# Kernel tuning notes

Measured on AMD Instinct MI355X. Metric: run time of the kernel, lower is better.

The kernel has to match this reference:

```python
import jax, jax.numpy as jnp
import numpy as np

K = 16  # neighbors per point (init kwarg k)


def setup_inputs() -> dict:
    key = jax.random.key(0)
    k0, k1, k2 = jax.random.split(key, 3)
    B, N, C, L, O = 4, 8192, 32, 64, 128
    return {
        "x": jax.random.normal(k0, (B, N, C), dtype=jnp.float32),
        "W_lin": jax.random.normal(k1, (C, L), dtype=jnp.float32) * 0.1,
        "b_lin": jnp.zeros((L,), dtype=jnp.float32),
        "W_conv": jax.random.normal(k2, (L, O), dtype=jnp.float32) * 0.1,
        "b_conv": jnp.zeros((O,), dtype=jnp.float32),
    }


def reference(x, W_lin, b_lin, W_conv, b_conv):
    # --- knn(x, k): squared-euclidean pairwise distance + top-k nearest ---
    sq = jnp.sum(x * x, axis=-1)                                   # [B,N]
    # dist[b,i,j] = ||x_i - x_j||^2  (self included, dist 0)
    dist = sq[:, :, None] - 2.0 * jnp.einsum('bnc,bmc->bnm', x, x) + sq[:, None, :]
    _, idx = jax.lax.top_k(-dist, K)                               # [B,N,K] int32
    # --- index_points: gather neighbor features ---
    knn_x = jax.vmap(lambda xb, ib: xb[ib])(x, idx)                # [B,N,K,C]
    # --- max pool over neighbors ---
    pooled = jnp.max(knn_x, axis=2)                                # [B,N,C]
    # --- Dense(linear) -> Conv1D(out_channel, kernel_size=1) -> relu ---
    h = pooled @ W_lin + b_lin                                     # [B,N,64]
    h = h @ W_conv + b_conv                                        # [B,N,128]
    return jax.nn.relu(h)
```

## Files before the change

kernel.cpp:

```cpp
#include <hip/hip_runtime.h>

#define NPTS   8192
#define CCH    32
#define LDIM   64
#define ODIM   128
#define KNN    16
#define QPB    64
#define TILEC  128
#define NTIL   (NPTS / TILEC)
#define NBLK   ((4 * NPTS) / QPB)
#define SCAP   57
#define MARGIN 0.75f
#define T32STR 65

typedef _Float16 half8   __attribute__((ext_vector_type(8)));
typedef float    float4v __attribute__((ext_vector_type(4)));

#define LDS_BYTES 54016
#define OFF_SQ   8192
#define OFF_SL   34816
#define OFF_SC   49408
#define OFF_TQ   49664
#define OFF_KN   49920
#define OFF_HH   8704

__device__ __forceinline__ void gload_lds16(const void* g, void* l) {
    __builtin_amdgcn_global_load_lds(
        (const __attribute__((address_space(1))) unsigned int*)g,
        (__attribute__((address_space(3))) unsigned int*)l, 16, 0, 0);
}
__device__ __forceinline__ void gload_lds4(const void* g, void* l) {
    __builtin_amdgcn_global_load_lds(
        (const __attribute__((address_space(1))) unsigned int*)g,
        (__attribute__((address_space(3))) unsigned int*)l, 4, 0, 0);
}

__global__ __launch_bounds__(256)
void prep_kernel(const float* __restrict__ x, float* __restrict__ sqg,
                 _Float16* __restrict__ xh) {
    __shared__ float lx[128 * 33];
    const int r = blockIdx.x;
    const int t = threadIdx.x;
    const float* src = x + (size_t)r * 4096;

    #pragma unroll
    for (int i = 0; i < 4; ++i) {
        int f4 = t + i * 256;
        float4 v = ((const float4*)src)[f4];
        int f = f4 * 4, pt = f >> 5, ch = f & 31;
        float* d = lx + pt * 33 + ch;
        d[0] = v.x; d[1] = v.y; d[2] = v.z; d[3] = v.w;
    }
    __syncthreads();
    if (t < 128) {
        const float* row = lx + t * 33;
        float s = 0.f;
        #pragma unroll
        for (int k = 0; k < 8; ++k) {
            float a = row[4*k], b = row[4*k+1], c = row[4*k+2], d = row[4*k+3];
            s += a * a + b * b + c * c + d * d;
        }
        sqg[r * 128 + t] = s;
    }
    char* rec = (char*)xh + (size_t)r * 8192;
    #pragma unroll
    for (int i = 0; i < 2; ++i) {
        int s2 = t * 2 + i;
        int st = s2 >> 6, q = (s2 >> 4) & 3, col = s2 & 15;
        const float* row = lx + (st * 16 + col) * 33 + q * 8;
        half8 h;
        #pragma unroll
        for (int j = 0; j < 8; ++j) h[j] = (_Float16)row[j];
        *(half8*)(rec + s2 * 16) = h;
    }
}

__global__ __launch_bounds__(512, 4)
void graph_layer_kernel(const float* __restrict__ x,
                        const float* __restrict__ sqg,
                        const _Float16* __restrict__ xh,
                        const float* __restrict__ Wl,
                        const float* __restrict__ bl,
                        const float* __restrict__ Wc,
                        const float* __restrict__ bc,
                        float* __restrict__ out)
{
    __shared__ __align__(16) char smem[LDS_BYTES];
    int*   slist = (int*)(smem + OFF_SL);
    float* t32   = (float*)smem;
    int*   scnt  = (int*)(smem + OFF_SC);
    float* tq    = (float*)(smem + OFF_TQ);
    float* skeys = (float*)smem;
    int*   kn    = (int*)(smem + OFF_KN);
    float* pl    = (float*)smem;
    float* hh    = (float*)(smem + OFF_HH);

    const int tid  = threadIdx.x;
    const int lane = tid & 63;
    const int w    = tid >> 6;
    const int g    = w >> 2;
    const int lw   = w & 3;
    const int col  = lane & 15;
    const int quad = lane >> 4;
    const float INF = __builtin_inff();

    const int bid = blockIdx.x;
    const int xcd = bid & 7, ixc = bid >> 3;
    const int vb  = ((xcd >> 1) << 7) | ((xcd & 1) << 6) | ixc;

    const int qb0 = vb * QPB;
    const int b   = qb0 >> 13;
    const int qbl = qb0 & (NPTS - 1);
    const int S   = vb & 31;
    const float* xb  = x   + (size_t)(b << 13) * CCH;
    const float* sqb = sqg + (b << 13);
    const char*  xhb = (const char*)xh + (size_t)b * NTIL * 8192;

    half8 qh;
    {
        int p = qb0 + lw * 16 + col;
        qh = *(const half8*)((const char*)xh
              + (size_t)(p >> 7) * 8192 + ((p >> 4) & 7) * 1024
              + quad * 256 + (p & 15) * 16);
    }

    auto tileof = [&](int I) { return (((I + S) & 31) << 1) | g; };
    auto bufat  = [&](int I) { return smem + (((g << 1) | (I & 1)) * 8704); };

    auto stage = [&](int I) {
        char* sb = bufat(I);
        int tile = tileof(I);
        const char* src = xhb + (size_t)tile * 8192;
        int tg = tid & 255;
        gload_lds16(src + tg * 16,        sb + lw * 1024);
        gload_lds16(src + 4096 + tg * 16, sb + 4096 + lw * 1024);
        if (lw < 2)
            gload_lds4(sqb + tile * TILEC + lw * 64 + lane, sb + OFF_SQ + lw * 256);
    };

    float m1[4] = {INF, INF, INF, INF};
    float m2[4] = {INF, INF, INF, INF};

    stage(0);
    __syncthreads();
    #pragma unroll 1
    for (int I = 0; I < 32; ++I) {
        if (I + 1 < 32) stage(I + 1);
        const char*  cb = bufat(I);
        const float* sv = (const float*)(cb + OFF_SQ);
        #pragma unroll
        for (int st = 0; st < 8; ++st) {
            half8 bh = *(const half8*)(cb + st * 1024 + lane * 16);
            float sc = sv[st * 16 + col];
            float4v acc = __builtin_amdgcn_mfma_f32_16x16x32_f16(
                qh, bh, (float4v){0.f, 0.f, 0.f, 0.f}, 0, 0, 0);
            #pragma unroll
            for (int j = 0; j < 4; ++j) {
                float key = fmaf(-2.f, acc[j], sc);
                float o1  = m1[j];
                m1[j] = fminf(key, o1);
                m2[j] = __builtin_amdgcn_fmed3f(key, o1, m2[j]);
            }
        }
        __syncthreads();
    }

    #pragma unroll
    for (int j = 0; j < 4; ++j) {
        int qq = lw * 16 + quad * 4 + j;
        t32[qq * T32STR + g * 32 + col * 2 + 0] = m1[j];
        t32[qq * T32STR + g * 32 + col * 2 + 1] = m2[j];
    }
    __syncthreads();
    {
        int q  = tid & 63;
        int wt = tid >> 6;
        float v[8]; int r[8];
        #pragma unroll
        for (int u = 0; u < 8; ++u) { v[u] = t32[q * T32STR + wt * 8 + u]; r[u] = 0; }
        #pragma unroll 8
        for (int jj = 0; jj < 64; ++jj) {
            float vj = t32[q * T32STR + jj];
            #pragma unroll
            for (int u = 0; u < 8; ++u)
                r[u] += (int)(vj < v[u]) | ((int)(vj == v[u]) & (int)(jj < wt * 8 + u));
        }
        #pragma unroll
        for (int u = 0; u < 8; ++u)
            if (r[u] == KNN - 1) tq[q] = v[u];
        if (tid < QPB) scnt[tid] = 0;
    }
    __syncthreads();
    float T2[4];
    #pragma unroll
    for (int j = 0; j < 4; ++j) T2[j] = tq[lw * 16 + quad * 4 + j] + MARGIN;

    stage(0);
    __syncthreads();
    #pragma unroll 1
    for (int I = 0; I < 32; ++I) {
        if (I + 1 < 32) stage(I + 1);
        const char*  cb = bufat(I);
        const float* sv = (const float*)(cb + OFF_SQ);
        int tbase = tileof(I) * TILEC;
        #pragma unroll
        for (int st = 0; st < 8; ++st) {
            half8 bh = *(const half8*)(cb + st * 1024 + lane * 16);
            float sc = sv[st * 16 + col];
            float4v acc = __builtin_amdgcn_mfma_f32_16x16x32_f16(
                qh, bh, (float4v){0.f, 0.f, 0.f, 0.f}, 0, 0, 0);
            #pragma unroll
            for (int j = 0; j < 4; ++j) {
                float key = fmaf(-2.f, acc[j], sc);
                if (key < T2[j]) {
                    int qq = lw * 16 + quad * 4 + j;
                    int slot = atomicAdd(&scnt[qq], 1);
                    if (slot < SCAP)
                        slist[qq * SCAP + slot] = tbase + st * 16 + col;
                }
            }
        }
        __syncthreads();
    }

    {
        int qq = tid & 63, sb8 = tid >> 6;
        int n = scnt[qq]; if (n > SCAP) n = SCAP;
        const float4* xi4 = (const float4*)(xb + (size_t)(qbl + qq) * CCH);
        for (int s = sb8; s < n; s += 8) {
            int jdx = slist[qq * SCAP + s];
            const float4* xj = (const float4*)(xb + (size_t)jdx * CCH);
            float a0 = 0.f, a1 = 0.f, a2 = 0.f, a3 = 0.f;
            #pragma unroll 2
            for (int k = 0; k < 8; ++k) {
                float4 cv = xj[k], qv = xi4[k];
                a0 = fmaf(cv.x, qv.x, a0); a1 = fmaf(cv.y, qv.y, a1);
                a2 = fmaf(cv.z, qv.z, a2); a3 = fmaf(cv.w, qv.w, a3);
            }
            float dot = (a0 + a1) + (a2 + a3);
            skeys[qq * SCAP + s] = fmaf(-2.f, dot, sqb[jdx]);
        }
    }
    __syncthreads();
    {
        int q  = tid & 63;
        int wt = tid >> 6;
        int n = scnt[q]; if (n > SCAP) n = SCAP;
        for (int s = wt; s < n; s += 8) {
            float k = skeys[q * SCAP + s];
            int   i = slist[q * SCAP + s];
            int rank = 0;
            #pragma unroll 4
            for (int jj = 0; jj < n; ++jj) {
                float kj = skeys[q * SCAP + jj];
                int   ij = slist[q * SCAP + jj];
                rank += (int)(kj < k) | ((int)(kj == k) & (int)(ij < i));
            }
            if (rank < KNN) kn[q * KNN + rank] = i;
        }
    }
    __syncthreads();

    {
        int q = tid >> 3, part = tid & 7;
        float4 m0 = make_float4(-INF, -INF, -INF, -INF);
        #pragma unroll 4
        for (int k = 0; k < KNN; ++k) {
            int j = kn[q * KNN + k];
            float4 v = *(const float4*)(xb + (size_t)j * CCH + part * 4);
            m0.x = fmaxf(m0.x, v.x); m0.y = fmaxf(m0.y, v.y);
            m0.z = fmaxf(m0.z, v.z); m0.w = fmaxf(m0.w, v.w);
        }
        float* d = pl + q * 33 + part * 4;
        d[0] = m0.x; d[1] = m0.y; d[2] = m0.z; d[3] = m0.w;
    }
    __syncthreads();
    {
        int l = tid & 63, qg2 = tid >> 6;
        #pragma unroll 1
        for (int qq = qg2; qq < QPB; qq += 8) {
            float acc = bl[l];
            #pragma unroll 8
            for (int c = 0; c < CCH; ++c)
                acc = fmaf(pl[qq * 33 + c], Wl[c * LDIM + l], acc);
            hh[qq * 65 + l] = acc;
        }
    }
    __syncthreads();
    {
        int o = tid & 127, qh2 = tid >> 7;
        #pragma unroll 1
        for (int qq = qh2; qq < QPB; qq += 4) {
            float acc = bc[o];
            #pragma unroll 8
            for (int l = 0; l < LDIM; ++l)
                acc = fmaf(hh[qq * 65 + l], Wc[l * ODIM + o], acc);
            out[(size_t)(qb0 + qq) * ODIM + o] = fmaxf(acc, 0.f);
        }
    }
}

extern "C" void kernel_launch(void* const* d_in, const int* in_sizes, int n_in,
                              void* d_out, int out_size, void* d_ws, size_t ws_size,
                              hipStream_t stream) {
    const float* x  = (const float*)d_in[0];
    const float* Wl = (const float*)d_in[1];
    const float* bl = (const float*)d_in[2];
    const float* Wc = (const float*)d_in[3];
    const float* bc = (const float*)d_in[4];
    float* out = (float*)d_out;
    float*    sqf = (float*)d_ws;
    _Float16* xh  = (_Float16*)((char*)d_ws + 131072);
    (void)in_sizes; (void)n_in; (void)out_size; (void)ws_size;

    hipLaunchKernelGGL(prep_kernel, dim3(256), dim3(256), 0, stream, x, sqf, xh);
    hipLaunchKernelGGL(graph_layer_kernel, dim3(NBLK), dim3(512), 0, stream,
                       x, sqf, xh, Wl, bl, Wc, bc, out);
}
```

Baseline: 235.6 us.

## Triple-buffer candidate tiles with partial vmcnt waits instead of full syncs

Replaces the double-buffered LDS staging of candidate tiles in both distance passes with a three-deep ring. Each wave issues the load two tiles ahead and waits only with s_waitcnt vmcnt(3) plus a raw s_barrier, rather than draining all loads through __syncthreads. The sq staging is now split so every wave loads 32 floats, which keeps the per-wave load count uniform for the vmcnt arithmetic. The cost is more LDS (about 71KB per block instead of 54KB), which may lower occupancy. It also stages tiles past index 31, which wrap around through tileof and are loaded redundantly.

```diff
diff --git a/kernel.cpp b/kernel.cpp
--- a/kernel.cpp
+++ b/kernel.cpp
@@ -16,12 +16,12 @@
 typedef _Float16 half8   __attribute__((ext_vector_type(8)));
 typedef float    float4v __attribute__((ext_vector_type(4)));
 
-#define LDS_BYTES 54016
+#define LDS_BYTES 71424
 #define OFF_SQ   8192
-#define OFF_SL   34816
-#define OFF_SC   49408
-#define OFF_TQ   49664
-#define OFF_KN   49920
+#define OFF_SL   52224
+#define OFF_SC   66816
+#define OFF_TQ   67072
+#define OFF_KN   67328
 #define OFF_HH   8704
 
 __device__ __forceinline__ void gload_lds16(const void* g, void* l) {
@@ -123,47 +123,55 @@
               + (size_t)(p >> 7) * 8192 + ((p >> 4) & 7) * 1024
               + quad * 256 + (p & 15) * 16);
     }
+    asm volatile("s_waitcnt vmcnt(0)" ::: "memory");
 
     auto tileof = [&](int I) { return (((I + S) & 31) << 1) | g; };
-    auto bufat  = [&](int I) { return smem + (((g << 1) | (I & 1)) * 8704); };
-
-    auto stage = [&](int I) {
-        char* sb = bufat(I);
+
+    auto stage_to = [&](char* sb, int I) {
         int tile = tileof(I);
         const char* src = xhb + (size_t)tile * 8192;
         int tg = tid & 255;
         gload_lds16(src + tg * 16,        sb + lw * 1024);
         gload_lds16(src + 4096 + tg * 16, sb + 4096 + lw * 1024);
-        if (lw < 2)
-            gload_lds4(sqb + tile * TILEC + lw * 64 + lane, sb + OFF_SQ + lw * 256);
+        if (lane < 32)
+            gload_lds4(sqb + tile * TILEC + lw * 32 + lane, sb + OFF_SQ + lw * 128);
     };
 
     float m1[4] = {INF, INF, INF, INF};
     float m2[4] = {INF, INF, INF, INF};
 
-    stage(0);
-    __syncthreads();
-    #pragma unroll 1
-    for (int I = 0; I < 32; ++I) {
-        if (I + 1 < 32) stage(I + 1);
-        const char*  cb = bufat(I);
-        const float* sv = (const float*)(cb + OFF_SQ);
-        #pragma unroll
-        for (int st = 0; st < 8; ++st) {
-            half8 bh = *(const half8*)(cb + st * 1024 + lane * 16);
-            float sc = sv[st * 16 + col];
-            float4v acc = __builtin_amdgcn_mfma_f32_16x16x32_f16(
-                qh, bh, (float4v){0.f, 0.f, 0.f, 0.f}, 0, 0, 0);
+    {
+        char* base = smem + g * 26112;
+        char *p0 = base, *p1 = base + 8704, *p2 = base + 17408;
+        stage_to(p0, 0); stage_to(p1, 1);
+        asm volatile("s_waitcnt vmcnt(3)" ::: "memory");
+        __builtin_amdgcn_s_barrier();
+        __builtin_amdgcn_sched_barrier(0);
+        #pragma unroll 1
+        for (int I = 0; I < 32; ++I) {
+            stage_to(p2, I + 2);
+            const float* sv = (const float*)(p0 + OFF_SQ);
             #pragma unroll
-            for (int j = 0; j < 4; ++j) {
-                float key = fmaf(-2.f, acc[j], sc);
-                float o1  = m1[j];
-                m1[j] = fminf(key, o1);
-                m2[j] = __builtin_amdgcn_fmed3f(key, o1, m2[j]);
+            for (int st = 0; st < 8; ++st) {
+                half8 bh = *(const half8*)(p0 + st * 1024 + lane * 16);
+                float sc = sv[st * 16 + col];
+                float4v acc = __builtin_amdgcn_mfma_f32_16x16x32_f16(
+                    qh, bh, (float4v){0.f, 0.f, 0.f, 0.f}, 0, 0, 0);
+                #pragma unroll
+                for (int j = 0; j < 4; ++j) {
+                    float key = fmaf(-2.f, acc[j], sc);
+                    float o1  = m1[j];
+                    m1[j] = fminf(key, o1);
+                    m2[j] = __builtin_amdgcn_fmed3f(key, o1, m2[j]);
+                }
             }
-        }
-        __syncthreads();
-    }
+            asm volatile("s_waitcnt vmcnt(3)" ::: "memory");
+            __builtin_amdgcn_s_barrier();
+            __builtin_amdgcn_sched_barrier(0);
+            char* t_ = p0; p0 = p1; p1 = p2; p2 = t_;
+        }
+    }
+    __syncthreads();
 
     #pragma unroll
     for (int j = 0; j < 4; ++j) {
@@ -195,33 +203,42 @@
     #pragma unroll
     for (int j = 0; j < 4; ++j) T2[j] = tq[lw * 16 + quad * 4 + j] + MARGIN;
 
-    stage(0);
-    __syncthreads();
-    #pragma unroll 1
-    for (int I = 0; I < 32; ++I) {
-        if (I + 1 < 32) stage(I + 1);
-        const char*  cb = bufat(I);
-        const float* sv = (const float*)(cb + OFF_SQ);
-        int tbase = tileof(I) * TILEC;
-        #pragma unroll
-        for (int st = 0; st < 8; ++st) {
-            half8 bh = *(const half8*)(cb + st * 1024 + lane * 16);
-            float sc = sv[st * 16 + col];
-            float4v acc = __builtin_amdgcn_mfma_f32_16x16x32_f16(
-                qh, bh, (float4v){0.f, 0.f, 0.f, 0.f}, 0, 0, 0);
+    {
+        char* base = smem + g * 26112;
+        char *p0 = base, *p1 = base + 8704, *p2 = base + 17408;
+        stage_to(p0, 0); stage_to(p1, 1);
+        asm volatile("s_waitcnt vmcnt(3)" ::: "memory");
+        __builtin_amdgcn_s_barrier();
+        __builtin_amdgcn_sched_barrier(0);
+        #pragma unroll 1
+        for (int I = 0; I < 32; ++I) {
+            stage_to(p2, I + 2);
+            const float* sv = (const float*)(p0 + OFF_SQ);
+            int tbase = tileof(I) * TILEC;
             #pragma unroll
-            for (int j = 0; j < 4; ++j) {
-                float key = fmaf(-2.f, acc[j], sc);
-                if (key < T2[j]) {
-                    int qq = lw * 16 + quad * 4 + j;
-                    int slot = atomicAdd(&scnt[qq], 1);
-                    if (slot < SCAP)
-                        slist[qq * SCAP + slot] = tbase + st * 16 + col;
+            for (int st = 0; st < 8; ++st) {
+                half8 bh = *(const half8*)(p0 + st * 1024 + lane * 16);
+                float sc = sv[st * 16 + col];
+                float4v acc = __builtin_amdgcn_mfma_f32_16x16x32_f16(
+                    qh, bh, (float4v){0.f, 0.f, 0.f, 0.f}, 0, 0, 0);
+                #pragma unroll
+                for (int j = 0; j < 4; ++j) {
+                    float key = fmaf(-2.f, acc[j], sc);
+                    if (key < T2[j]) {
+                        int qq = lw * 16 + quad * 4 + j;
+                        int slot = atomicAdd(&scnt[qq], 1);
+                        if (slot < SCAP)
+                            slist[qq * SCAP + slot] = tbase + st * 16 + col;
+                    }
                 }
             }
-        }
-        __syncthreads();
-    }
+            asm volatile("s_waitcnt vmcnt(3)" ::: "memory");
+            __builtin_amdgcn_s_barrier();
+            __builtin_amdgcn_sched_barrier(0);
+            char* t_ = p0; p0 = p1; p1 = p2; p2 = t_;
+        }
+    }
+    __syncthreads();
 
     {
         int qq = tid & 63, sb8 = tid >> 6;
```

Result: no change. 234.7 us (-0.4%).
